# Performance work log

Hardware: AMD Instinct MI355X
Metric: run time of the kernel (lower is better)

The kernel has to match this reference:

```python
import jax, jax.numpy as jnp
import numpy as np

B, T, D_MODEL, D_HEAD = 4, 2048, 1024, 64

def setup_inputs() -> dict:
    key = jax.random.key(0)
    k1, k2, k3, k4 = jax.random.split(key, 4)
    x = jax.random.normal(k1, (B, T, D_MODEL), dtype=jnp.float32)
    # Linear(d_model, d_head) weights stored as [d_model, d_head] for x @ W
    s = 1.0 / np.sqrt(D_MODEL)
    W_Q = jax.random.normal(k2, (D_MODEL, D_HEAD), dtype=jnp.float32) * s
    W_K = jax.random.normal(k3, (D_MODEL, D_HEAD), dtype=jnp.float32) * s
    W_V = jax.random.normal(k4, (D_MODEL, D_HEAD), dtype=jnp.float32) * s
    return {"x": x, "W_Q": W_Q, "W_K": W_K, "W_V": W_V}

def reference(x, W_Q, W_K, W_V):
    d_head = W_Q.shape[-1]
    Q = jnp.einsum('btm,md->btd', x, W_Q)
    K = jnp.einsum('btm,md->btd', x, W_K)
    V = jnp.einsum('btm,md->btd', x, W_V)
    A = jnp.einsum('bid,bjd->bij', Q, K) / jnp.sqrt(jnp.asarray(d_head, x.dtype))
    T_ = x.shape[1]
    causal = jnp.tril(jnp.ones((T_, T_), dtype=bool))  # [T, T]
    A = jnp.where(causal, A, -jnp.inf)
    A = jax.nn.softmax(A, axis=-1)
    return jnp.einsum('bij,bjd->bid', A, V)
```

## Files before the change

kernel.cpp:

```cpp
#include <hip/hip_runtime.h>
#include <hip/hip_bf16.h>

#define NB 4
#define NT 2048
#define DM 1024
#define DH 64

typedef __attribute__((ext_vector_type(8))) short bf16x8;
typedef __attribute__((ext_vector_type(4))) float f32x4;
typedef unsigned short u16;
typedef unsigned int u32;

static __device__ __forceinline__ u16 f2b(float f) {
    __hip_bfloat16 h = __float2bfloat16(f);
    return __builtin_bit_cast(u16, h);
}
static __device__ __forceinline__ float b2f(u16 h) {
    return __builtin_bit_cast(float, (u32)h << 16);
}
static __device__ __forceinline__ void gld16(const void* g, void* l) {
    __builtin_amdgcn_global_load_lds((const __attribute__((address_space(1))) void*)g,
                                     (__attribute__((address_space(3))) void*)l, 16, 0, 0);
}
#define BAR() __builtin_amdgcn_s_barrier()
#define SBAR() __builtin_amdgcn_sched_barrier(0)

__global__ __launch_bounds__(256) void wt_conv(
    const float* __restrict__ WQ, const float* __restrict__ WK,
    const float* __restrict__ WV, u16* __restrict__ wt)
{
    __shared__ u16 tl[64][68];
    const int which = blockIdx.y, kt = blockIdx.x;
    const float* W = (which == 0) ? WQ : (which == 1) ? WK : WV;
    #pragma unroll
    for (int i = 0; i < 4; ++i) {
        int r = (threadIdx.x >> 4) + i * 16;
        int c = (threadIdx.x & 15) * 4;
        float4 v = *(const float4*)&W[(size_t)(kt * 64 + r) * DH + c];
        tl[r][c] = f2b(v.x); tl[r][c + 1] = f2b(v.y);
        tl[r][c + 2] = f2b(v.z); tl[r][c + 3] = f2b(v.w);
    }
    __syncthreads();
    int d = threadIdx.x >> 2, kc = (threadIdx.x & 3) * 16;
    u16 buf[16];
    #pragma unroll
    for (int j = 0; j < 16; ++j) buf[j] = tl[kc + j][d];
    u16* dst = wt + which * 65536 + d * 1024 + kt * 64 + kc;
    *(uint4*)dst = *(uint4*)&buf[0];
    *(uint4*)(dst + 8) = *(uint4*)&buf[8];
}

__global__ __launch_bounds__(256) void qkv_gemm(
    const float* __restrict__ x, const u16* __restrict__ wt,
    u16* __restrict__ Qb, u16* __restrict__ Kb, u16* __restrict__ Vt)
{
    __shared__ float xs[2][4096];
    __shared__ u16 wsm[2][4096];
    const int tid = threadIdx.x, lane = tid & 63, w = tid >> 6;
    const int l15 = lane & 15, g = lane >> 4;
    const int row0 = blockIdx.x * 64;
    const int which = blockIdx.y;
    const u16* Wg = wt + which * 65536;

    auto stage = [&](int kt, int bi) {
        #pragma unroll
        for (int i = 0; i < 4; ++i) {
            u32 D = (u32)(w * 4096 + i * 1024 + lane * 16);
            u32 r = D >> 8, c = D & 255;
            u32 cs = c ^ ((r & 7) << 5);
            gld16(x + (size_t)(row0 + r) * DM + kt * 64 + (cs >> 2),
                  (char*)&xs[bi][0] + w * 4096 + i * 1024);
        }
        #pragma unroll
        for (int i = 0; i < 2; ++i) {
            u32 D = (u32)(w * 2048 + i * 1024 + lane * 16);
            u32 r = D >> 7, c = D & 127;
            u32 cs = c ^ ((r & 7) << 4);
            gld16(Wg + (size_t)r * 1024 + kt * 64 + (cs >> 1),
                  (char*)&wsm[bi][0] + w * 2048 + i * 1024);
        }
    };

    f32x4 acc[4];
    #pragma unroll
    for (int i = 0; i < 4; ++i) acc[i] = {0.f, 0.f, 0.f, 0.f};

    stage(0, 0);

    const int arow = w * 16 + l15;
    #pragma unroll
    for (int kt = 0; kt < 16; ++kt) {
        if (kt < 15) {
            stage(kt + 1, (kt + 1) & 1);
            asm volatile("s_waitcnt vmcnt(6)" ::: "memory");
        } else {
            asm volatile("s_waitcnt vmcnt(0)" ::: "memory");
        }
        BAR();
        SBAR();
        const char* xb = (const char*)&xs[kt & 1][0];
        const char* wb = (const char*)&wsm[kt & 1][0];
        #pragma unroll
        for (int ks = 0; ks < 2; ++ks) {
            u32 abase = (u32)(arow * 256 + ks * 128 + g * 32);
            f32x4 a0 = *(const f32x4*)(xb + (abase ^ ((arow & 7) << 5)));
            f32x4 a1 = *(const f32x4*)(xb + ((abase + 16) ^ ((arow & 7) << 5)));
            bf16x8 afrag;
            #pragma unroll
            for (int e = 0; e < 4; ++e) afrag[e] = (short)f2b(a0[e]);
            #pragma unroll
            for (int e = 0; e < 4; ++e) afrag[4 + e] = (short)f2b(a1[e]);
            __builtin_amdgcn_s_setprio(1);
            #pragma unroll
            for (int nt = 0; nt < 4; ++nt) {
                int brow = nt * 16 + l15;
                u32 bb = (u32)(brow * 128 + ks * 64 + g * 16);
                bf16x8 bfrag = *(const bf16x8*)(wb + (bb ^ ((brow & 7) << 4)));
                acc[nt] = __builtin_amdgcn_mfma_f32_16x16x32_bf16(afrag, bfrag, acc[nt], 0, 0, 0);
            }
            __builtin_amdgcn_s_setprio(0);
        }
        BAR();
    }
    #pragma unroll
    for (int nt = 0; nt < 4; ++nt) {
        int dcol = nt * 16 + l15;
        #pragma unroll
        for (int r = 0; r < 4; ++r) {
            int row = row0 + w * 16 + g * 4 + r;
            float v = acc[nt][r];
            if (which == 0)      Qb[(size_t)row * DH + dcol] = f2b(v * 0.125f);
            else if (which == 1) Kb[(size_t)row * DH + dcol] = f2b(v);
            else { int bb2 = row >> 11, t = row & 2047;
                   Vt[(size_t)bb2 * DH * NT + (size_t)dcol * NT + t] = f2b(v); }
        }
    }
}

__global__ __launch_bounds__(256) void attn(
    const u16* __restrict__ Qb, const u16* __restrict__ Kb,
    const u16* __restrict__ Vt, u16* __restrict__ pOt, float* __restrict__ pml,
    int CHUNK, int SLOTS)
{
    __shared__ u16 k_lds[2][4096];
    __shared__ u16 v_lds[2][4096];
    __shared__ f32x4 p_lds[4][128];

    const int tid = threadIdx.x, lane = tid & 63, w = tid >> 6;
    const int l15 = lane & 15, g = lane >> 4;
    const int b = blockIdx.y;

    int flat = blockIdx.x, qb = 0, nc;
    for (;;) { nc = (qb + CHUNK) / CHUNK; if (flat < nc) break; flat -= nc; ++qb; }
    const int chunk = flat;
    const int t0 = chunk * CHUNK;
    const int t1 = min(t0 + CHUNK, qb + 1);
    const int q0 = qb * 64;

    const u16* Qg = Qb + ((size_t)b * NT + q0 + w * 16) * DH;
    const u16* Kg = Kb + (size_t)b * NT * DH;
    const u16* Vg = Vt + (size_t)b * DH * NT;

    auto stage = [&](int t, int bi) {
        const int j0 = t * 64;
        #pragma unroll
        for (int i = 0; i < 2; ++i) {
            u32 D = (u32)(w * 2048 + i * 1024 + lane * 16);
            u32 r = D >> 7, c = D & 127;
            u32 cs = c ^ ((r & 7) << 4);
            gld16(Kg + (size_t)(j0 + r) * DH + (cs >> 1),
                  (char*)&k_lds[bi][0] + w * 2048 + i * 1024);
            gld16(Vg + (size_t)r * NT + j0 + (cs >> 1),
                  (char*)&v_lds[bi][0] + w * 2048 + i * 1024);
        }
    };

    stage(t0, 0);

    bf16x8 qf[2];
    qf[0] = *(const bf16x8*)(Qg + l15 * DH + g * 8);
    qf[1] = *(const bf16x8*)(Qg + l15 * DH + 32 + g * 8);

    float m_run = -INFINITY, l_run = 0.f;
    f32x4 oacc[4];
    #pragma unroll
    for (int nt = 0; nt < 4; ++nt) oacc[nt] = {0.f, 0.f, 0.f, 0.f};

    char* pw = (char*)&p_lds[w][0];
    const int swz = (l15 & 7) << 4;

    for (int t = t0; t < t1; ++t) {
        const int cur = (t - t0) & 1;
        if (t + 1 < t1) {
            stage(t + 1, cur ^ 1);
            asm volatile("s_waitcnt vmcnt(4)" ::: "memory");
        } else {
            asm volatile("s_waitcnt vmcnt(0)" ::: "memory");
        }
        BAR();
        SBAR();
        const char* kb = (const char*)&k_lds[cur][0];
        const char* vb = (const char*)&v_lds[cur][0];

        f32x4 sacc[4];
        #pragma unroll
        for (int nt = 0; nt < 4; ++nt) sacc[nt] = {0.f, 0.f, 0.f, 0.f};
        __builtin_amdgcn_s_setprio(1);
        #pragma unroll
        for (int ks = 0; ks < 2; ++ks) {
            #pragma unroll
            for (int nt = 0; nt < 4; ++nt) {
                int arow = nt * 16 + l15;
                u32 aa = (u32)(arow * 128 + ks * 64 + g * 16);
                bf16x8 kf = *(const bf16x8*)(kb + (aa ^ ((arow & 7) << 4)));
                sacc[nt] = __builtin_amdgcn_mfma_f32_16x16x32_bf16(kf, qf[ks], sacc[nt], 0, 0, 0);
            }
        }
        __builtin_amdgcn_s_setprio(0);
        if (t == qb) {
            const int q_local = w * 16 + l15;
            #pragma unroll
            for (int nt = 0; nt < 4; ++nt)
                #pragma unroll
                for (int r = 0; r < 4; ++r)
                    if (nt * 16 + g * 4 + r > q_local) sacc[nt][r] = -1e30f;
        }
        float mx = -INFINITY;
        #pragma unroll
        for (int nt = 0; nt < 4; ++nt) {
            float a = fmaxf(fmaxf(sacc[nt][0], sacc[nt][1]),
                            fmaxf(sacc[nt][2], sacc[nt][3]));
            mx = fmaxf(mx, a);
        }
        mx = fmaxf(mx, __shfl_xor(mx, 16));
        mx = fmaxf(mx, __shfl_xor(mx, 32));
        const float m_new = fmaxf(m_run, mx);
        const float alpha = __expf(m_run - m_new);
        float p[4][4];
        float ps = 0.f;
        #pragma unroll
        for (int nt = 0; nt < 4; ++nt)
            #pragma unroll
            for (int r = 0; r < 4; ++r) {
                float pv = __expf(sacc[nt][r] - m_new);
                p[nt][r] = pv; ps += pv;
            }
        ps += __shfl_xor(ps, 16);
        ps += __shfl_xor(ps, 32);
        l_run = l_run * alpha + ps;
        m_run = m_new;
        #pragma unroll
        for (int nt = 0; nt < 4; ++nt)
            #pragma unroll
            for (int r = 0; r < 4; ++r) oacc[nt][r] *= alpha;

        #pragma unroll
        for (int nt = 0; nt < 4; ++nt) {
            uint2 pk;
            pk.x = (u32)f2b(p[nt][0]) | ((u32)f2b(p[nt][1]) << 16);
            pk.y = (u32)f2b(p[nt][2]) | ((u32)f2b(p[nt][3]) << 16);
            u32 a = (u32)((l15 * 128 + nt * 32 + g * 8) ^ swz);
            *(uint2*)(pw + a) = pk;
        }
        bf16x8 pb[2];
        #pragma unroll
        for (int ks = 0; ks < 2; ++ks)
            pb[ks] = *(const bf16x8*)(pw + ((u32)(l15 * 128 + ks * 64 + g * 16) ^ swz));

        __builtin_amdgcn_s_setprio(1);
        #pragma unroll
        for (int ks = 0; ks < 2; ++ks) {
            #pragma unroll
            for (int nt = 0; nt < 4; ++nt) {
                int arow = nt * 16 + l15;
                u32 aa = (u32)(arow * 128 + ks * 64 + g * 16);
                bf16x8 vf = *(const bf16x8*)(vb + (aa ^ ((arow & 7) << 4)));
                oacc[nt] = __builtin_amdgcn_mfma_f32_16x16x32_bf16(vf, pb[ks], oacc[nt], 0, 0, 0);
            }
        }
        __builtin_amdgcn_s_setprio(0);
        BAR();
    }

    const int slot = (b * 32 + qb) * SLOTS + chunk;
    u16* Op = pOt + (size_t)slot * 4096;
    #pragma unroll
    for (int nt = 0; nt < 4; ++nt)
        #pragma unroll
        for (int r = 0; r < 4; ++r)
            Op[(nt * 16 + g * 4 + r) * 64 + w * 16 + l15] = f2b(oacc[nt][r]);
    if (g == 0) {
        float* mlp = pml + (size_t)slot * 128;
        mlp[(w * 16 + l15) * 2]     = m_run;
        mlp[(w * 16 + l15) * 2 + 1] = l_run;
    }
}

__global__ __launch_bounds__(256) void merge(
    const u16* __restrict__ pOt, const float* __restrict__ pml,
    float* __restrict__ out, int CHUNK, int SLOTS)
{
    __shared__ float tl[64][65];
    const int bq = blockIdx.x;
    const int b = bq >> 5, qb = bq & 31;
    const int nc = (qb + CHUNK) / CHUNK;
    const int base = bq * SLOTS;
    const int q = threadIdx.x & 63, ds = threadIdx.x >> 6;

    float m = -INFINITY;
    for (int c = 0; c < nc; ++c)
        m = fmaxf(m, pml[(size_t)(base + c) * 128 + q * 2]);
    float lsum = 0.f;
    float acc[16];
    #pragma unroll
    for (int i = 0; i < 16; ++i) acc[i] = 0.f;
    for (int c = 0; c < nc; ++c) {
        const float mc = pml[(size_t)(base + c) * 128 + q * 2];
        const float lc = pml[(size_t)(base + c) * 128 + q * 2 + 1];
        const float wc = __expf(mc - m);
        lsum += wc * lc;
        const u16* Op = pOt + (size_t)(base + c) * 4096;
        #pragma unroll
        for (int i = 0; i < 16; ++i)
            acc[i] += wc * b2f(Op[(ds * 16 + i) * 64 + q]);
    }
    const float inv = 1.f / lsum;
    #pragma unroll
    for (int i = 0; i < 16; ++i) tl[q][ds * 16 + i] = acc[i] * inv;
    __syncthreads();
    const int q2 = threadIdx.x >> 2, dc = threadIdx.x & 3;
    float* orow = out + ((size_t)b * NT + qb * 64 + q2) * 64 + dc * 16;
    #pragma unroll
    for (int j4 = 0; j4 < 4; ++j4) {
        float4 v = { tl[q2][dc * 16 + j4 * 4 + 0], tl[q2][dc * 16 + j4 * 4 + 1],
                     tl[q2][dc * 16 + j4 * 4 + 2], tl[q2][dc * 16 + j4 * 4 + 3] };
        *(float4*)&orow[j4 * 4] = v;
    }
}

extern "C" void kernel_launch(void* const* d_in, const int* in_sizes, int n_in,
                              void* d_out, int out_size, void* d_ws, size_t ws_size,
                              hipStream_t stream) {
    const float* x  = (const float*)d_in[0];
    const float* WQ = (const float*)d_in[1];
    const float* WK = (const float*)d_in[2];
    const float* WV = (const float*)d_in[3];
    float* out = (float*)d_out;

    char* ws = (char*)d_ws;
    u16* Qb = (u16*)ws;
    u16* Kb = (u16*)(ws + 1048576);
    u16* Vt = (u16*)(ws + 2097152);
    u16* Wt = (u16*)(ws + 3145728);
    int CHUNK, SLOTS;
    if (ws_size >= 9830400) { CHUNK = 6;  SLOTS = 6; }
    else                    { CHUNK = 16; SLOTS = 2; }
    u16*   pOt = (u16*)(ws + 3145728);
    float* pml = (float*)(ws + 3145728 + (size_t)NB * 32 * SLOTS * 4096 * 2);

    int gx = 0;
    for (int qb = 0; qb < 32; ++qb) gx += (qb + CHUNK) / CHUNK;

    wt_conv<<<dim3(16, 3), 256, 0, stream>>>(WQ, WK, WV, Wt);
    qkv_gemm<<<dim3(128, 3), 256, 0, stream>>>(x, Wt, Qb, Kb, Vt);
    attn<<<dim3(gx, NB), 256, 0, stream>>>(Qb, Kb, Vt, pOt, pml, CHUNK, SLOTS);
    merge<<<NB * 32, 256, 0, stream>>>(pOt, pml, out, CHUNK, SLOTS);
}
```

Baseline: 45.62 us.

## Widen attention KV tile to 128 keys and fix split chunking

The attention kernel now processes 128 keys per iteration instead of 64, with a wider V-transpose LDS layout and swizzle, a larger P buffer, and a diagonal mask offset for 64-row query blocks. Chunk splitting is hard-coded to 3 tiles of 128 keys with 6 slots, the grid is fixed at 102 blocks per batch, and pOt is moved past the weight buffer. The intent is fewer barriers and softmax passes per key, plus more MFMA work per stage. The cost is double the LDS footprint, more registers, and wasted masked work on the diagonal tile. The workspace size is no longer checked before use.

```diff
diff --git a/kernel.cpp b/kernel.cpp
--- a/kernel.cpp
+++ b/kernel.cpp
@@ -5,6 +5,8 @@
 #define NT 2048
 #define DM 1024
 #define DH 64
+#define CHUNK3 3
+#define SLOTS 6
 
 typedef __attribute__((ext_vector_type(8))) short bf16x8;
 typedef __attribute__((ext_vector_type(4))) float f32x4;
@@ -139,22 +141,28 @@
 
 __global__ __launch_bounds__(256) void attn(
     const u16* __restrict__ Qb, const u16* __restrict__ Kb,
-    const u16* __restrict__ Vt, u16* __restrict__ pOt, float* __restrict__ pml,
-    int CHUNK, int SLOTS)
+    const u16* __restrict__ Vt, u16* __restrict__ pOt, float* __restrict__ pml)
 {
-    __shared__ u16 k_lds[2][4096];
-    __shared__ u16 v_lds[2][4096];
-    __shared__ f32x4 p_lds[4][128];
+    __shared__ u16 k_lds[2][8192];
+    __shared__ u16 v_lds[2][8192];
+    __shared__ f32x4 p_lds[4][256];
 
     const int tid = threadIdx.x, lane = tid & 63, w = tid >> 6;
     const int l15 = lane & 15, g = lane >> 4;
     const int b = blockIdx.y;
 
-    int flat = blockIdx.x, qb = 0, nc;
-    for (;;) { nc = (qb + CHUNK) / CHUNK; if (flat < nc) break; flat -= nc; ++qb; }
+    int flat = blockIdx.x, qb = 0, nc, nt128;
+    for (;;) {
+        nt128 = (qb + 2) >> 1;
+        nc = (nt128 + CHUNK3 - 1) / CHUNK3;
+        if (flat < nc) break;
+        flat -= nc; ++qb;
+    }
     const int chunk = flat;
-    const int t0 = chunk * CHUNK;
-    const int t1 = min(t0 + CHUNK, qb + 1);
+    const int t0 = chunk * CHUNK3;
+    const int t1 = min(t0 + CHUNK3, nt128);
+    const int tD = nt128 - 1;
+    const int delta = qb * 64 - tD * 128;
     const int q0 = qb * 64;
 
     const u16* Qg = Qb + ((size_t)b * NT + q0 + w * 16) * DH;
@@ -162,19 +170,24 @@
     const u16* Vg = Vt + (size_t)b * DH * NT;
 
     auto stage = [&](int t, int bi) {
-        const int j0 = t * 64;
-        #pragma unroll
-        for (int i = 0; i < 2; ++i) {
-            u32 D = (u32)(w * 2048 + i * 1024 + lane * 16);
-            u32 r = D >> 7, c = D & 127;
-            u32 cs = c ^ ((r & 7) << 4);
-            gld16(Kg + (size_t)(j0 + r) * DH + (cs >> 1),
-                  (char*)&k_lds[bi][0] + w * 2048 + i * 1024);
-            gld16(Vg + (size_t)r * NT + j0 + (cs >> 1),
-                  (char*)&v_lds[bi][0] + w * 2048 + i * 1024);
+        const int j0 = t * 128;
+        #pragma unroll
+        for (int i = 0; i < 4; ++i) {
+            u32 D = (u32)(w * 4096 + i * 1024 + lane * 16);
+            {
+                u32 r = D >> 7, c = D & 127;
+                u32 cs = c ^ ((r & 7) << 4);
+                gld16(Kg + (size_t)(j0 + r) * DH + (cs >> 1),
+                      (char*)&k_lds[bi][0] + w * 4096 + i * 1024);
+            }
+            {
+                u32 r = D >> 8, c = D & 255;
+                u32 cs = c ^ ((r & 15) << 4);
+                gld16(Vg + (size_t)r * NT + j0 + (cs >> 1),
+                      (char*)&v_lds[bi][0] + w * 4096 + i * 1024);
+            }
         }
     };
-
     stage(t0, 0);
 
     bf16x8 qf[2];
@@ -187,13 +200,14 @@
     for (int nt = 0; nt < 4; ++nt) oacc[nt] = {0.f, 0.f, 0.f, 0.f};
 
     char* pw = (char*)&p_lds[w][0];
-    const int swz = (l15 & 7) << 4;
+    const u32 pswz = (u32)((l15 & 15) << 4);
+    const int q_local = w * 16 + l15;
 
     for (int t = t0; t < t1; ++t) {
         const int cur = (t - t0) & 1;
         if (t + 1 < t1) {
             stage(t + 1, cur ^ 1);
-            asm volatile("s_waitcnt vmcnt(4)" ::: "memory");
+            asm volatile("s_waitcnt vmcnt(8)" ::: "memory");
         } else {
             asm volatile("s_waitcnt vmcnt(0)" ::: "memory");
         }
@@ -202,48 +216,47 @@
         const char* kb = (const char*)&k_lds[cur][0];
         const char* vb = (const char*)&v_lds[cur][0];
 
-        f32x4 sacc[4];
-        #pragma unroll
-        for (int nt = 0; nt < 4; ++nt) sacc[nt] = {0.f, 0.f, 0.f, 0.f};
+        f32x4 sacc[8];
+        #pragma unroll
+        for (int f = 0; f < 8; ++f) sacc[f] = {0.f, 0.f, 0.f, 0.f};
         __builtin_amdgcn_s_setprio(1);
         #pragma unroll
         for (int ks = 0; ks < 2; ++ks) {
             #pragma unroll
-            for (int nt = 0; nt < 4; ++nt) {
-                int arow = nt * 16 + l15;
+            for (int f = 0; f < 8; ++f) {
+                int arow = f * 16 + l15;
                 u32 aa = (u32)(arow * 128 + ks * 64 + g * 16);
                 bf16x8 kf = *(const bf16x8*)(kb + (aa ^ ((arow & 7) << 4)));
-                sacc[nt] = __builtin_amdgcn_mfma_f32_16x16x32_bf16(kf, qf[ks], sacc[nt], 0, 0, 0);
+                sacc[f] = __builtin_amdgcn_mfma_f32_16x16x32_bf16(kf, qf[ks], sacc[f], 0, 0, 0);
             }
         }
         __builtin_amdgcn_s_setprio(0);
-        if (t == qb) {
-            const int q_local = w * 16 + l15;
-            #pragma unroll
-            for (int nt = 0; nt < 4; ++nt)
+        if (t == tD) {
+            #pragma unroll
+            for (int f = 0; f < 8; ++f)
                 #pragma unroll
                 for (int r = 0; r < 4; ++r)
-                    if (nt * 16 + g * 4 + r > q_local) sacc[nt][r] = -1e30f;
+                    if (f * 16 + g * 4 + r > delta + q_local) sacc[f][r] = -1e30f;
         }
         float mx = -INFINITY;
         #pragma unroll
-        for (int nt = 0; nt < 4; ++nt) {
-            float a = fmaxf(fmaxf(sacc[nt][0], sacc[nt][1]),
-                            fmaxf(sacc[nt][2], sacc[nt][3]));
+        for (int f = 0; f < 8; ++f) {
+            float a = fmaxf(fmaxf(sacc[f][0], sacc[f][1]),
+                            fmaxf(sacc[f][2], sacc[f][3]));
             mx = fmaxf(mx, a);
         }
         mx = fmaxf(mx, __shfl_xor(mx, 16));
         mx = fmaxf(mx, __shfl_xor(mx, 32));
         const float m_new = fmaxf(m_run, mx);
         const float alpha = __expf(m_run - m_new);
-        float p[4][4];
+        float p[8][4];
         float ps = 0.f;
         #pragma unroll
-        for (int nt = 0; nt < 4; ++nt)
+        for (int f = 0; f < 8; ++f)
             #pragma unroll
             for (int r = 0; r < 4; ++r) {
-                float pv = __expf(sacc[nt][r] - m_new);
-                p[nt][r] = pv; ps += pv;
+                float pv = __expf(sacc[f][r] - m_new);
+                p[f][r] = pv; ps += pv;
             }
         ps += __shfl_xor(ps, 16);
         ps += __shfl_xor(ps, 32);
@@ -255,27 +268,27 @@
             for (int r = 0; r < 4; ++r) oacc[nt][r] *= alpha;
 
         #pragma unroll
-        for (int nt = 0; nt < 4; ++nt) {
+        for (int f = 0; f < 8; ++f) {
             uint2 pk;
-            pk.x = (u32)f2b(p[nt][0]) | ((u32)f2b(p[nt][1]) << 16);
-            pk.y = (u32)f2b(p[nt][2]) | ((u32)f2b(p[nt][3]) << 16);
-            u32 a = (u32)((l15 * 128 + nt * 32 + g * 8) ^ swz);
+            pk.x = (u32)f2b(p[f][0]) | ((u32)f2b(p[f][1]) << 16);
+            pk.y = (u32)f2b(p[f][2]) | ((u32)f2b(p[f][3]) << 16);
+            u32 a = (u32)(l15 * 256 + f * 32 + g * 8) ^ pswz;
             *(uint2*)(pw + a) = pk;
         }
-        bf16x8 pb[2];
-        #pragma unroll
-        for (int ks = 0; ks < 2; ++ks)
-            pb[ks] = *(const bf16x8*)(pw + ((u32)(l15 * 128 + ks * 64 + g * 16) ^ swz));
+        bf16x8 pb_[4];
+        #pragma unroll
+        for (int ksj = 0; ksj < 4; ++ksj)
+            pb_[ksj] = *(const bf16x8*)(pw + ((u32)(l15 * 256 + ksj * 64 + g * 16) ^ pswz));
 
         __builtin_amdgcn_s_setprio(1);
         #pragma unroll
-        for (int ks = 0; ks < 2; ++ks) {
+        for (int ksj = 0; ksj < 4; ++ksj) {
             #pragma unroll
             for (int nt = 0; nt < 4; ++nt) {
                 int arow = nt * 16 + l15;
-                u32 aa = (u32)(arow * 128 + ks * 64 + g * 16);
-                bf16x8 vf = *(const bf16x8*)(vb + (aa ^ ((arow & 7) << 4)));
-                oacc[nt] = __builtin_amdgcn_mfma_f32_16x16x32_bf16(vf, pb[ks], oacc[nt], 0, 0, 0);
+                u32 aa = (u32)(arow * 256 + ksj * 64 + g * 16);
+                bf16x8 vf = *(const bf16x8*)(vb + (aa ^ ((arow & 15) << 4)));
+                oacc[nt] = __builtin_amdgcn_mfma_f32_16x16x32_bf16(vf, pb_[ksj], oacc[nt], 0, 0, 0);
             }
         }
         __builtin_amdgcn_s_setprio(0);
@@ -298,12 +311,13 @@
 
 __global__ __launch_bounds__(256) void merge(
     const u16* __restrict__ pOt, const float* __restrict__ pml,
-    float* __restrict__ out, int CHUNK, int SLOTS)
+    float* __restrict__ out)
 {
     __shared__ float tl[64][65];
     const int bq = blockIdx.x;
     const int b = bq >> 5, qb = bq & 31;
-    const int nc = (qb + CHUNK) / CHUNK;
+    const int nt128 = (qb + 2) >> 1;
+    const int nc = (nt128 + CHUNK3 - 1) / CHUNK3;
     const int base = bq * SLOTS;
     const int q = threadIdx.x & 63, ds = threadIdx.x >> 6;
 
@@ -348,21 +362,15 @@
     float* out = (float*)d_out;
 
     char* ws = (char*)d_ws;
-    u16* Qb = (u16*)ws;
-    u16* Kb = (u16*)(ws + 1048576);
-    u16* Vt = (u16*)(ws + 2097152);
-    u16* Wt = (u16*)(ws + 3145728);
-    int CHUNK, SLOTS;
-    if (ws_size >= 9830400) { CHUNK = 6;  SLOTS = 6; }
-    else                    { CHUNK = 16; SLOTS = 2; }
-    u16*   pOt = (u16*)(ws + 3145728);
-    float* pml = (float*)(ws + 3145728 + (size_t)NB * 32 * SLOTS * 4096 * 2);
-
-    int gx = 0;
-    for (int qb = 0; qb < 32; ++qb) gx += (qb + CHUNK) / CHUNK;
+    u16*   Qb  = (u16*)ws;
+    u16*   Kb  = (u16*)(ws + 1048576);
+    u16*   Vt  = (u16*)(ws + 2097152);
+    u16*   Wt  = (u16*)(ws + 3145728);
+    u16*   pOt = (u16*)(ws + 3538944);
+    float* pml = (float*)(ws + 3538944 + 6291456);
 
     wt_conv<<<dim3(16, 3), 256, 0, stream>>>(WQ, WK, WV, Wt);
     qkv_gemm<<<dim3(128, 3), 256, 0, stream>>>(x, Wt, Qb, Kb, Vt);
-    attn<<<dim3(gx, NB), 256, 0, stream>>>(Qb, Kb, Vt, pOt, pml, CHUNK, SLOTS);
-    merge<<<NB * 32, 256, 0, stream>>>(pOt, pml, out, CHUNK, SLOTS);
-}
+    attn<<<dim3(102, NB), 256, 0, stream>>>(Qb, Kb, Vt, pOt, pml);
+    merge<<<NB * 32, 256, 0, stream>>>(pOt, pml, out);
+}
```

Result: faster. 42.79 us (-6.2%).
